# Performance work log

Measured on AMD Instinct MI355X. Metric: run time of the kernel, lower is better.

Reference implementation:

```python
import jax, jax.numpy as jnp
import numpy as np

N_NODES = 100000
N_EDGES = 300000
NUM_GRAPHS = 2000
IN_DIM = 82
HIDDEN = 256


def _gcn_conv(x, src, dst, dinv, W, b):
    # GCNConv: out = D^-1/2 (A + I) D^-1/2 (x W) + b
    xW = x @ W  # [N, H]
    norm = dinv[src] * dinv[dst]  # [E]
    agg = jax.ops.segment_sum(xW[src] * norm[:, None], dst, num_segments=N_NODES)
    self_loop = xW * (dinv * dinv)[:, None]
    return agg + self_loop + b


def setup_inputs() -> dict:
    key = jax.random.key(0)
    ks = jax.random.split(key, 8)
    x = jax.random.normal(ks[0], (N_NODES, IN_DIM), dtype=jnp.float32)
    edge_index = jax.random.randint(ks[1], (2, N_EDGES), 0, N_NODES, dtype=jnp.int64)
    batch = jnp.sort(jax.random.randint(ks[2], (N_NODES,), 0, NUM_GRAPHS, dtype=jnp.int64))
    W1 = jax.random.normal(ks[3], (IN_DIM, HIDDEN), dtype=jnp.float32) * (1.0 / np.sqrt(IN_DIM))
    W2 = jax.random.normal(ks[4], (HIDDEN, HIDDEN), dtype=jnp.float32) * (1.0 / np.sqrt(HIDDEN))
    W3 = jax.random.normal(ks[5], (HIDDEN, HIDDEN), dtype=jnp.float32) * (1.0 / np.sqrt(HIDDEN))
    b1 = jnp.zeros((HIDDEN,), jnp.float32)
    b2 = jnp.zeros((HIDDEN,), jnp.float32)
    b3 = jnp.zeros((HIDDEN,), jnp.float32)
    return {"x": x, "edge_index": edge_index, "batch": batch, "num_graphs": NUM_GRAPHS,
            "W1": W1, "b1": b1, "W2": W2, "b2": b2, "W3": W3, "b3": b3}


def reference(x, edge_index, batch, num_graphs, W1, b1, W2, b2, W3, b3):
    src, dst = edge_index[0], edge_index[1]
    # symmetric normalization with added self-loops (PyG gcn_norm)
    deg = jax.ops.segment_sum(jnp.ones_like(dst, dtype=x.dtype), dst, num_segments=N_NODES) + 1.0
    dinv = jax.lax.rsqrt(deg)
    h = jax.nn.relu(_gcn_conv(x, src, dst, dinv, W1, b1))
    h = jax.nn.relu(_gcn_conv(h, src, dst, dinv, W2, b2))
    h = jax.nn.relu(_gcn_conv(h, src, dst, dinv, W3, b3))
    return jax.ops.segment_max(h, batch, num_segments=num_graphs)  # [G, H]
```

## Files before the change

kernel.cpp:

```cpp
#include <hip/hip_runtime.h>
#include <cstdint>
#include <cstddef>

#define N_NODES 100000
#define N_EDGES 300000
#define N_GRAPHS 2000
#define HID 256
#define INDIM 82
#define XCPAD 84
#define K1PAD 128
#define N_TILES ((N_NODES + 255) / 256)
#define SCAN_CHUNK 2048
#define NBLK_SCAN ((N_NODES + SCAN_CHUNK - 1) / SCAN_CHUNK)

typedef __bf16 bf16x8 __attribute__((ext_vector_type(8)));
typedef float f32x4 __attribute__((ext_vector_type(4)));

__device__ __forceinline__ unsigned short f2bf(float f) {
    union { __bf16 h; unsigned short u; } v;
    v.h = (__bf16)f;
    return v.u;
}
__device__ __forceinline__ float bf2f(unsigned short s) {
    return __uint_as_float(((unsigned int)s) << 16);
}

__global__ void k_cnt_acc(const int* __restrict__ ei, int* cnt) {
    int e = blockIdx.x * 256 + threadIdx.x;
    if (e < N_EDGES) atomicAdd(&cnt[ei[N_EDGES + e]], 1);
}

__global__ __launch_bounds__(256) void k_scan1(const int* __restrict__ cnt, int* __restrict__ off,
                                               int* __restrict__ partial) {
    __shared__ int sdata[256];
    const int base = blockIdx.x * SCAN_CHUNK;
    const int t = threadIdx.x;
    int v[8];
    int s = 0;
#pragma unroll
    for (int i = 0; i < 8; ++i) {
        int idx = base + t * 8 + i;
        v[i] = (idx < N_NODES) ? cnt[idx] : 0;
        s += v[i];
    }
    sdata[t] = s;
    __syncthreads();
    for (int d = 1; d < 256; d <<= 1) {
        int x = (t >= d) ? sdata[t - d] : 0;
        __syncthreads();
        sdata[t] += x;
        __syncthreads();
    }
    int run = sdata[t] - s;
#pragma unroll
    for (int i = 0; i < 8; ++i) {
        int idx = base + t * 8 + i;
        if (idx < N_NODES) off[idx] = run;
        run += v[i];
    }
    if (t == 255) partial[blockIdx.x] = sdata[255];
}

__global__ void k_scan2(int* partial) {
    if (threadIdx.x == 0 && blockIdx.x == 0) {
        int run = 0;
        for (int i = 0; i < NBLK_SCAN; ++i) {
            int v = partial[i];
            partial[i] = run;
            run += v;
        }
    }
}

__global__ void k_scan3(int* __restrict__ off, const int* __restrict__ partial,
                        int* __restrict__ cur, const int* __restrict__ cnt,
                        float* __restrict__ dinv) {
    int i = blockIdx.x * 256 + threadIdx.x;
    if (i < N_NODES) {
        int o = off[i] + partial[i >> 11];
        off[i] = o;
        cur[i] = o;
        dinv[i] = rsqrtf((float)cnt[i] + 1.0f);
    }
}

__global__ void k_fill(const int* __restrict__ ei, const float* __restrict__ dinv, int* cur,
                       int* __restrict__ csr_src, float* __restrict__ csr_norm) {
    int e = blockIdx.x * 256 + threadIdx.x;
    if (e < N_EDGES) {
        int s = ei[e];
        int d = ei[N_EDGES + e];
        int pos = atomicAdd(&cur[d], 1);
        csr_src[pos] = s;
        csr_norm[pos] = dinv[s] * dinv[d];
    }
}

__device__ __forceinline__ void wconv_body(const float* __restrict__ W,
                                           unsigned short* __restrict__ Wb, int KSRC, int i) {
    int kc = i >> 13;
    int r = i & 8191;
    int nt = r >> 9;
    int r2 = r & 511;
    int lg = r2 >> 7;
    int lr = (r2 >> 3) & 15;
    int j = r2 & 7;
    int k = kc * 32 + lg * 8 + j;
    int n = nt * 16 + lr;
    Wb[i] = (k < KSRC) ? f2bf(W[(size_t)k * HID + n]) : (unsigned short)0;
}

#define PREP_W1 128
#define PREP_W23 256
#define PREP_BND 8
#define PREP_XC ((N_NODES * XCPAD + 255) / 256)
#define PREP_BLOCKS (PREP_W1 + 2 * PREP_W23 + PREP_BND + PREP_XC)

__global__ void k_prep(const float* __restrict__ x, unsigned short* __restrict__ xc,
                       const float* __restrict__ W1, unsigned short* __restrict__ Wb1,
                       const float* __restrict__ W2, unsigned short* __restrict__ Wb2,
                       const float* __restrict__ W3, unsigned short* __restrict__ Wb3,
                       const int* __restrict__ batch, int* __restrict__ gstart) {
    int b = blockIdx.x;
    int t = threadIdx.x;
    if (b < PREP_W1) { wconv_body(W1, Wb1, INDIM, b * 256 + t); return; }
    b -= PREP_W1;
    if (b < PREP_W23) { wconv_body(W2, Wb2, HID, b * 256 + t); return; }
    b -= PREP_W23;
    if (b < PREP_W23) { wconv_body(W3, Wb3, HID, b * 256 + t); return; }
    b -= PREP_W23;
    if (b < PREP_BND) {
        int g = b * 256 + t;
        if (g <= N_GRAPHS) {
            int lo = 0, hi = N_NODES;
            while (lo < hi) {
                int mid = (lo + hi) >> 1;
                if (batch[mid] < g) lo = mid + 1;
                else hi = mid;
            }
            gstart[g] = lo;
        }
        return;
    }
    b -= PREP_BND;
    int i = b * 256 + t;
    if (i < N_NODES * XCPAD) {
        int node = i / XCPAD;
        int k = i - node * XCPAD;
        xc[i] = (k < INDIM) ? f2bf(x[(size_t)node * INDIM + k]) : (unsigned short)0;
    }
}

template <int K>
__global__ __launch_bounds__(512) void k_gemm_mfma(const unsigned short* __restrict__ A,
                                                   const unsigned short* __restrict__ Wb,
                                                   const float* __restrict__ bias,
                                                   unsigned short* __restrict__ Cb) {
    constexpr int NK = K / 32;
    __shared__ __align__(16) unsigned short Wsh[K * HID];

    const int tid = threadIdx.x;
    const int w = tid >> 6;
    const int l = tid & 63;
    const int lr = l & 15;
    const int lg = l >> 4;

#pragma unroll
    for (int i = 0; i < K / 16; ++i) {
        int o = (i * 512 + tid) * 8;
        *reinterpret_cast<uint4*>(&Wsh[o]) = *reinterpret_cast<const uint4*>(Wb + o);
    }
    __syncthreads();

    float bv[16];
#pragma unroll
    for (int nt = 0; nt < 16; ++nt) bv[nt] = bias[nt * 16 + lr];

    for (int t = blockIdx.x; t < N_TILES; t += 256) {
        const int rowbase = t * 256 + w * 32;
        int r0 = rowbase + lr;
        int r1 = rowbase + 16 + lr;
        int r0c = r0 < N_NODES ? r0 : (N_NODES - 1);
        int r1c = r1 < N_NODES ? r1 : (N_NODES - 1);
        const unsigned short* a0p = A + (size_t)r0c * K + lg * 8;
        const unsigned short* a1p = A + (size_t)r1c * K + lg * 8;

        bf16x8 a0[NK], a1[NK];
#pragma unroll
        for (int kc = 0; kc < NK; ++kc) {
            a0[kc] = *reinterpret_cast<const bf16x8*>(a0p + kc * 32);
            a1[kc] = *reinterpret_cast<const bf16x8*>(a1p + kc * 32);
        }

        f32x4 acc0[16] = {};
        f32x4 acc1[16] = {};

#pragma unroll
        for (int kc = 0; kc < NK; ++kc) {
            const unsigned short* bfp = Wsh + kc * 8192 + l * 8;
#pragma unroll
            for (int nt = 0; nt < 16; ++nt) {
                bf16x8 bb = *reinterpret_cast<const bf16x8*>(bfp + nt * 512);
                acc0[nt] = __builtin_amdgcn_mfma_f32_16x16x32_bf16(a0[kc], bb, acc0[nt], 0, 0, 0);
                acc1[nt] = __builtin_amdgcn_mfma_f32_16x16x32_bf16(a1[kc], bb, acc1[nt], 0, 0, 0);
            }
        }

        int gr0 = rowbase + lg * 4;
#pragma unroll
        for (int j = 0; j < 4; ++j) {
            int gr = gr0 + j;
            if (gr < N_NODES) {
                size_t base = (size_t)gr * HID + lr;
#pragma unroll
                for (int nt = 0; nt < 16; ++nt)
                    Cb[base + nt * 16] = f2bf(fmaxf(acc0[nt][j] + bv[nt], 0.0f));
            }
            int gr2 = gr + 16;
            if (gr2 < N_NODES) {
                size_t base = (size_t)gr2 * HID + lr;
#pragma unroll
                for (int nt = 0; nt < 16; ++nt)
                    Cb[base + nt * 16] = f2bf(fmaxf(acc1[nt][j] + bv[nt], 0.0f));
            }
        }
    }
}

__global__ void k_aggregate256(const unsigned short* __restrict__ tb,
                               const float* __restrict__ dinv, const int* __restrict__ off,
                               const int* __restrict__ cnt, const int* __restrict__ csr_src,
                               const float* __restrict__ csr_norm,
                               unsigned short* __restrict__ ob) {
    int node = blockIdx.x * 4 + (threadIdx.x >> 6);
    if (node >= N_NODES) return;
    int lane = threadIdx.x & 63;
    const size_t lo = (size_t)lane * 4;
    int o0 = off[node];
    int n = cnt[node];
    float di = dinv[node];
    float s2 = di * di;
    ushort4 sv = *reinterpret_cast<const ushort4*>(&tb[(size_t)node * HID + lo]);
    float4 acc = {bf2f(sv.x) * s2, bf2f(sv.y) * s2, bf2f(sv.z) * s2, bf2f(sv.w) * s2};

    int j = 0;
    for (; j + 3 < n; j += 4) {
        int s0 = csr_src[o0 + j];
        int s1 = csr_src[o0 + j + 1];
        int s2i = csr_src[o0 + j + 2];
        int s3 = csr_src[o0 + j + 3];
        float n0 = csr_norm[o0 + j];
        float n1 = csr_norm[o0 + j + 1];
        float n2 = csr_norm[o0 + j + 2];
        float n3 = csr_norm[o0 + j + 3];
        ushort4 u0 = *reinterpret_cast<const ushort4*>(&tb[(size_t)s0 * HID + lo]);
        ushort4 u1 = *reinterpret_cast<const ushort4*>(&tb[(size_t)s1 * HID + lo]);
        ushort4 u2 = *reinterpret_cast<const ushort4*>(&tb[(size_t)s2i * HID + lo]);
        ushort4 u3 = *reinterpret_cast<const ushort4*>(&tb[(size_t)s3 * HID + lo]);
        acc.x = fmaf(n0, bf2f(u0.x), acc.x); acc.y = fmaf(n0, bf2f(u0.y), acc.y);
        acc.z = fmaf(n0, bf2f(u0.z), acc.z); acc.w = fmaf(n0, bf2f(u0.w), acc.w);
        acc.x = fmaf(n1, bf2f(u1.x), acc.x); acc.y = fmaf(n1, bf2f(u1.y), acc.y);
        acc.z = fmaf(n1, bf2f(u1.z), acc.z); acc.w = fmaf(n1, bf2f(u1.w), acc.w);
        acc.x = fmaf(n2, bf2f(u2.x), acc.x); acc.y = fmaf(n2, bf2f(u2.y), acc.y);
        acc.z = fmaf(n2, bf2f(u2.z), acc.z); acc.w = fmaf(n2, bf2f(u2.w), acc.w);
        acc.x = fmaf(n3, bf2f(u3.x), acc.x); acc.y = fmaf(n3, bf2f(u3.y), acc.y);
        acc.z = fmaf(n3, bf2f(u3.z), acc.z); acc.w = fmaf(n3, bf2f(u3.w), acc.w);
    }
    int rem = n - j;
    if (rem & 2) {
        int s0 = csr_src[o0 + j];
        int s1 = csr_src[o0 + j + 1];
        float n0 = csr_norm[o0 + j];
        float n1 = csr_norm[o0 + j + 1];
        ushort4 u0 = *reinterpret_cast<const ushort4*>(&tb[(size_t)s0 * HID + lo]);
        ushort4 u1 = *reinterpret_cast<const ushort4*>(&tb[(size_t)s1 * HID + lo]);
        acc.x = fmaf(n0, bf2f(u0.x), acc.x); acc.y = fmaf(n0, bf2f(u0.y), acc.y);
        acc.z = fmaf(n0, bf2f(u0.z), acc.z); acc.w = fmaf(n0, bf2f(u0.w), acc.w);
        acc.x = fmaf(n1, bf2f(u1.x), acc.x); acc.y = fmaf(n1, bf2f(u1.y), acc.y);
        acc.z = fmaf(n1, bf2f(u1.z), acc.z); acc.w = fmaf(n1, bf2f(u1.w), acc.w);
        j += 2;
    }
    if (rem & 1) {
        int s0 = csr_src[o0 + j];
        float n0 = csr_norm[o0 + j];
        ushort4 u0 = *reinterpret_cast<const ushort4*>(&tb[(size_t)s0 * HID + lo]);
        acc.x = fmaf(n0, bf2f(u0.x), acc.x); acc.y = fmaf(n0, bf2f(u0.y), acc.y);
        acc.z = fmaf(n0, bf2f(u0.z), acc.z); acc.w = fmaf(n0, bf2f(u0.w), acc.w);
    }
    ushort4 o;
    o.x = f2bf(acc.x);
    o.y = f2bf(acc.y);
    o.z = f2bf(acc.z);
    o.w = f2bf(acc.w);
    *reinterpret_cast<ushort4*>(&ob[(size_t)node * HID + lo]) = o;
}

__global__ void k_aggx(const unsigned short* __restrict__ xc,
                       const float* __restrict__ dinv, const int* __restrict__ off,
                       const int* __restrict__ cnt, const int* __restrict__ csr_src,
                       const float* __restrict__ csr_norm,
                       unsigned short* __restrict__ ob) {
    int node = blockIdx.x * 4 + (threadIdx.x >> 6);
    if (node >= N_NODES) return;
    int lane = threadIdx.x & 63;
    const bool act = lane < (XCPAD / 2);
    const size_t co = (size_t)lane * 2;
    int o0 = off[node];
    int n = cnt[node];
    float di = dinv[node];
    float s2 = di * di;
    float2 acc = {0.0f, 0.0f};
    if (act) {
        ushort2 sv = *reinterpret_cast<const ushort2*>(&xc[(size_t)node * XCPAD + co]);
        acc.x = bf2f(sv.x) * s2;
        acc.y = bf2f(sv.y) * s2;
    }
    int j = 0;
    for (; j + 3 < n; j += 4) {
        int s0 = csr_src[o0 + j];
        int s1 = csr_src[o0 + j + 1];
        int s2i = csr_src[o0 + j + 2];
        int s3 = csr_src[o0 + j + 3];
        float n0 = csr_norm[o0 + j];
        float n1 = csr_norm[o0 + j + 1];
        float n2 = csr_norm[o0 + j + 2];
        float n3 = csr_norm[o0 + j + 3];
        if (act) {
            ushort2 u0 = *reinterpret_cast<const ushort2*>(&xc[(size_t)s0 * XCPAD + co]);
            ushort2 u1 = *reinterpret_cast<const ushort2*>(&xc[(size_t)s1 * XCPAD + co]);
            ushort2 u2 = *reinterpret_cast<const ushort2*>(&xc[(size_t)s2i * XCPAD + co]);
            ushort2 u3 = *reinterpret_cast<const ushort2*>(&xc[(size_t)s3 * XCPAD + co]);
            acc.x = fmaf(n0, bf2f(u0.x), acc.x); acc.y = fmaf(n0, bf2f(u0.y), acc.y);
            acc.x = fmaf(n1, bf2f(u1.x), acc.x); acc.y = fmaf(n1, bf2f(u1.y), acc.y);
            acc.x = fmaf(n2, bf2f(u2.x), acc.x); acc.y = fmaf(n2, bf2f(u2.y), acc.y);
            acc.x = fmaf(n3, bf2f(u3.x), acc.x); acc.y = fmaf(n3, bf2f(u3.y), acc.y);
        }
    }
    int rem = n - j;
    if (rem & 2) {
        int s0 = csr_src[o0 + j];
        int s1 = csr_src[o0 + j + 1];
        float n0 = csr_norm[o0 + j];
        float n1 = csr_norm[o0 + j + 1];
        if (act) {
            ushort2 u0 = *reinterpret_cast<const ushort2*>(&xc[(size_t)s0 * XCPAD + co]);
            ushort2 u1 = *reinterpret_cast<const ushort2*>(&xc[(size_t)s1 * XCPAD + co]);
            acc.x = fmaf(n0, bf2f(u0.x), acc.x); acc.y = fmaf(n0, bf2f(u0.y), acc.y);
            acc.x = fmaf(n1, bf2f(u1.x), acc.x); acc.y = fmaf(n1, bf2f(u1.y), acc.y);
        }
        j += 2;
    }
    if (rem & 1) {
        int s0 = csr_src[o0 + j];
        float n0 = csr_norm[o0 + j];
        if (act) {
            ushort2 u0 = *reinterpret_cast<const ushort2*>(&xc[(size_t)s0 * XCPAD + co]);
            acc.x = fmaf(n0, bf2f(u0.x), acc.x); acc.y = fmaf(n0, bf2f(u0.y), acc.y);
        }
    }
    ushort2 o;
    o.x = f2bf(acc.x);
    o.y = f2bf(acc.y);
    *reinterpret_cast<ushort2*>(&ob[(size_t)node * K1PAD + co]) = o;
}

__global__ void k_pool2(const unsigned short* __restrict__ hb, const int* __restrict__ gstart,
                        float* __restrict__ out) {
    int g = blockIdx.x;
    int w = threadIdx.x >> 6;
    int lane = threadIdx.x & 63;
    int col = w * 128 + lane * 2;
    int s = gstart[g], e = gstart[g + 1];
    float2 m = {0.0f, 0.0f};
    for (int i = s; i < e; ++i) {
        ushort2 u = *reinterpret_cast<const ushort2*>(&hb[(size_t)i * HID + col]);
        m.x = fmaxf(m.x, bf2f(u.x));
        m.y = fmaxf(m.y, bf2f(u.y));
    }
    *reinterpret_cast<float2*>(&out[(size_t)g * HID + col]) = m;
}

extern "C" void kernel_launch(void* const* d_in, const int* in_sizes, int n_in,
                              void* d_out, int out_size, void* d_ws, size_t ws_size,
                              hipStream_t stream) {
    const float* x = (const float*)d_in[0];
    const int* ei = (const int*)d_in[1];
    const int* batch = (const int*)d_in[2];
    const float* W1 = (const float*)d_in[4];
    const float* b1 = (const float*)d_in[5];
    const float* W2 = (const float*)d_in[6];
    const float* b2 = (const float*)d_in[7];
    const float* W3 = (const float*)d_in[8];
    const float* b3 = (const float*)d_in[9];
    float* out = (float*)d_out;

    char* ws = (char*)d_ws;
    float* dinv = (float*)(ws);
    int* cnt = (int*)(ws + (512 << 10));
    int* off = (int*)(ws + (1024 << 10));
    int* cur = (int*)(ws + (1536 << 10));
    int* part = (int*)(ws + (2048 << 10));
    int* gstart = (int*)(ws + (2048 << 10) + 4096);
    int* csr_src = (int*)(ws + (2176 << 10));
    float* csr_norm = (float*)(ws + (3392 << 10));
    unsigned short* Wb1 = (unsigned short*)(ws + (4608 << 10));
    unsigned short* Wb2 = (unsigned short*)(ws + (4736 << 10));
    unsigned short* Wb3 = (unsigned short*)(ws + (4928 << 10));
    unsigned short* ag1_b = (unsigned short*)(ws + (5120 << 10));
    unsigned short* bufA = (unsigned short*)(ws + (5120 << 10) + 25600000);
    unsigned short* bufB = (unsigned short*)(ws + (5120 << 10) + 76800000);
    unsigned short* x_c = (unsigned short*)(ws + (5120 << 10) + 128000000);

    const int nblk_edges = (N_EDGES + 255) / 256;
    const int nblk_nodes = (N_NODES + 255) / 256;
    const int nblk_rows4 = (N_NODES + 3) / 4;

    hipMemsetAsync(cnt, 0, N_NODES * sizeof(int), stream);
    k_cnt_acc<<<nblk_edges, 256, 0, stream>>>(ei, cnt);
    k_scan1<<<NBLK_SCAN, 256, 0, stream>>>(cnt, off, part);
    k_scan2<<<1, 64, 0, stream>>>(part);
    k_scan3<<<nblk_nodes, 256, 0, stream>>>(off, part, cur, cnt, dinv);
    k_fill<<<nblk_edges, 256, 0, stream>>>(ei, dinv, cur, csr_src, csr_norm);

    k_prep<<<PREP_BLOCKS, 256, 0, stream>>>(x, x_c, W1, Wb1, W2, Wb2, W3, Wb3, batch, gstart);

    k_aggx<<<nblk_rows4, 256, 0, stream>>>(x_c, dinv, off, cnt, csr_src, csr_norm, ag1_b);
    k_gemm_mfma<K1PAD><<<256, 512, 0, stream>>>(ag1_b, Wb1, b1, bufA);

    k_aggregate256<<<nblk_rows4, 256, 0, stream>>>(bufA, dinv, off, cnt, csr_src, csr_norm, bufB);
    k_gemm_mfma<HID><<<256, 512, 0, stream>>>(bufB, Wb2, b2, bufA);

    k_aggregate256<<<nblk_rows4, 256, 0, stream>>>(bufA, dinv, off, cnt, csr_src, csr_norm, bufB);
    k_gemm_mfma<HID><<<256, 512, 0, stream>>>(bufB, Wb3, b3, bufA);

    k_pool2<<<N_GRAPHS, 128, 0, stream>>>(bufA, gstart, out);
}
```

Before: 257.8 us.

## Permute hidden-column layout so GEMM epilogue writes contiguous 16-element rows

The GEMM epilogue now stores hidden features in a permuted column order (column nt*16+lr is placed at lr*16+nt), so each lane writes two 16-byte vector stores instead of sixteen scattered 2-byte stores. To keep results correct, the rows of W2 and W3 are permuted to match when converted, and the final pooling un-permutes columns on output. This adds layout bookkeeping across kernels, and the pool's final stores become scattered scalar writes.

```diff
diff --git a/kernel.cpp b/kernel.cpp
--- a/kernel.cpp
+++ b/kernel.cpp
@@ -24,6 +24,7 @@
 __device__ __forceinline__ float bf2f(unsigned short s) {
     return __uint_as_float(((unsigned int)s) << 16);
 }
+__device__ __forceinline__ int sig(int c) { return ((c & 15) << 4) | (c >> 4); }
 
 __global__ void k_cnt_acc(const int* __restrict__ ei, int* cnt) {
     int e = blockIdx.x * 256 + threadIdx.x;
@@ -97,7 +98,8 @@
 }
 
 __device__ __forceinline__ void wconv_body(const float* __restrict__ W,
-                                           unsigned short* __restrict__ Wb, int KSRC, int i) {
+                                           unsigned short* __restrict__ Wb, int KSRC, int i,
+                                           bool perm) {
     int kc = i >> 13;
     int r = i & 8191;
     int nt = r >> 9;
@@ -106,6 +108,7 @@
     int lr = (r2 >> 3) & 15;
     int j = r2 & 7;
     int k = kc * 32 + lg * 8 + j;
+    if (perm) k = sig(k);
     int n = nt * 16 + lr;
     Wb[i] = (k < KSRC) ? f2bf(W[(size_t)k * HID + n]) : (unsigned short)0;
 }
@@ -123,11 +126,11 @@
                        const int* __restrict__ batch, int* __restrict__ gstart) {
     int b = blockIdx.x;
     int t = threadIdx.x;
-    if (b < PREP_W1) { wconv_body(W1, Wb1, INDIM, b * 256 + t); return; }
+    if (b < PREP_W1) { wconv_body(W1, Wb1, INDIM, b * 256 + t, false); return; }
     b -= PREP_W1;
-    if (b < PREP_W23) { wconv_body(W2, Wb2, HID, b * 256 + t); return; }
+    if (b < PREP_W23) { wconv_body(W2, Wb2, HID, b * 256 + t, true); return; }
     b -= PREP_W23;
-    if (b < PREP_W23) { wconv_body(W3, Wb3, HID, b * 256 + t); return; }
+    if (b < PREP_W23) { wconv_body(W3, Wb3, HID, b * 256 + t, true); return; }
     b -= PREP_W23;
     if (b < PREP_BND) {
         int g = b * 256 + t;
@@ -211,17 +214,23 @@
         for (int j = 0; j < 4; ++j) {
             int gr = gr0 + j;
             if (gr < N_NODES) {
-                size_t base = (size_t)gr * HID + lr;
+                unsigned short t0[16];
 #pragma unroll
                 for (int nt = 0; nt < 16; ++nt)
-                    Cb[base + nt * 16] = f2bf(fmaxf(acc0[nt][j] + bv[nt], 0.0f));
+                    t0[nt] = f2bf(fmaxf(acc0[nt][j] + bv[nt], 0.0f));
+                unsigned short* p = Cb + (size_t)gr * HID + lr * 16;
+                *reinterpret_cast<uint4*>(p) = *reinterpret_cast<const uint4*>(t0);
+                *reinterpret_cast<uint4*>(p + 8) = *reinterpret_cast<const uint4*>(t0 + 8);
             }
             int gr2 = gr + 16;
             if (gr2 < N_NODES) {
-                size_t base = (size_t)gr2 * HID + lr;
+                unsigned short t1[16];
 #pragma unroll
                 for (int nt = 0; nt < 16; ++nt)
-                    Cb[base + nt * 16] = f2bf(fmaxf(acc1[nt][j] + bv[nt], 0.0f));
+                    t1[nt] = f2bf(fmaxf(acc1[nt][j] + bv[nt], 0.0f));
+                unsigned short* p = Cb + (size_t)gr2 * HID + lr * 16;
+                *reinterpret_cast<uint4*>(p) = *reinterpret_cast<const uint4*>(t1);
+                *reinterpret_cast<uint4*>(p + 8) = *reinterpret_cast<const uint4*>(t1 + 8);
             }
         }
     }
@@ -369,15 +378,16 @@
     int g = blockIdx.x;
     int w = threadIdx.x >> 6;
     int lane = threadIdx.x & 63;
-    int col = w * 128 + lane * 2;
+    int p = w * 128 + lane * 2;
     int s = gstart[g], e = gstart[g + 1];
     float2 m = {0.0f, 0.0f};
     for (int i = s; i < e; ++i) {
-        ushort2 u = *reinterpret_cast<const ushort2*>(&hb[(size_t)i * HID + col]);
+        ushort2 u = *reinterpret_cast<const ushort2*>(&hb[(size_t)i * HID + p]);
         m.x = fmaxf(m.x, bf2f(u.x));
         m.y = fmaxf(m.y, bf2f(u.y));
     }
-    *reinterpret_cast<float2*>(&out[(size_t)g * HID + col]) = m;
+    out[(size_t)g * HID + sig(p)] = m.x;
+    out[(size_t)g * HID + sig(p + 1)] = m.y;
 }
 
 extern "C" void kernel_launch(void* const* d_in, const int* in_sizes, int n_in,
```

Result: no change. 254.8 us (-1.1%).
